# Kernel optimization log

Measured on AMD Instinct MI355X. Metric: run time of the kernel, lower is better.

The kernel has to match this reference:

```python
import jax, jax.numpy as jnp
import numpy as np

TAO, M = 3, 5
C_IN, D_MODEL = 7, 512
KERNELS = D_MODEL // C_IN            # 73
LEFTOUT = D_MODEL - C_IN * KERNELS   # 1
KSIZE = 3
B, L = 32, 4096


def setup_inputs() -> dict:
    key = jax.random.key(0)
    k1, k2, k3, k4, k5 = jax.random.split(key, 5)
    x = jax.random.normal(k1, (B, L, C_IN), dtype=jnp.float32)
    fan_in = (M + 1) * KSIZE
    # kaiming_normal_(mode='fan_in', nonlinearity='leaky_relu', neg_slope=0.01)
    std = float(np.sqrt(2.0 / ((1.0 + 0.01 ** 2) * fan_in)))
    conv_w = jax.random.normal(k2, (KERNELS, M + 1, KSIZE), dtype=jnp.float32) * std
    bb = float(1.0 / np.sqrt(fan_in))  # torch default conv bias init: U(-1/sqrt(fan_in), +)
    conv_b = jax.random.uniform(k3, (KERNELS,), minval=-bb, maxval=bb, dtype=jnp.float32)
    leftout_w = jax.random.normal(k4, (LEFTOUT, M + 1, KSIZE), dtype=jnp.float32) * std
    leftout_b = jax.random.uniform(k5, (LEFTOUT,), minval=-bb, maxval=bb, dtype=jnp.float32)
    return {"x": x, "conv_w": conv_w, "conv_b": conv_b,
            "leftout_w": leftout_w, "leftout_b": leftout_b}


def _circ_conv(inp, w, b):
    # inp: [N, M+1, L]; circular padding=1, kernel 3, 'VALID' after wrap pad
    inp_c = jnp.pad(inp, ((0, 0), (0, 0), (1, 1)), mode="wrap")
    out = jax.lax.conv_general_dilated(
        inp_c, w, window_strides=(1,), padding="VALID",
        dimension_numbers=("NCH", "OIH", "NCH"))
    return out + b[None, :, None]


def reference(x, conv_w, conv_b, leftout_w, leftout_b):
    Bb, Ll, c = x.shape
    off = M * TAO
    # faithful-vector gather: for t in [off, L), take x[t - i*tao, c_], c-major then i
    idx = jnp.arange(off, Ll)[:, None] - jnp.arange(M + 1)[None, :] * TAO  # [L', M+1]
    g = x[:, idx, :]                                   # [B, L', M+1, c]
    g = jnp.transpose(g, (0, 1, 3, 2)).reshape(Bb, Ll - off, c * (M + 1))
    emb = jnp.pad(g, ((0, 0), (off, 0), (0, 0)))       # pad front of seq -> [B, L, c*(M+1)]
    # split into c chunks of (M+1) channels; fold chunk dim into batch for shared conv
    inp = emb.reshape(Bb, Ll, c, M + 1).transpose(0, 2, 3, 1).reshape(Bb * c, M + 1, Ll)
    out = _circ_conv(inp, conv_w, conv_b)              # [B*c, KERNELS, L]
    pieces = out.reshape(Bb, c * KERNELS, Ll)
    if LEFTOUT > 0:
        last = inp.reshape(Bb, c, M + 1, Ll)[:, -1]    # last chunk's conv input [B, M+1, L]
        extra = _circ_conv(last, leftout_w, leftout_b)  # [B, LEFTOUT, L]
        pieces = jnp.concatenate([pieces, extra], axis=1)
    return jnp.transpose(pieces, (0, 2, 1))            # [B, L, d_model]
```

## Files before the change

### kernel.cpp

```cpp
#include <hip/hip_runtime.h>

#define C_IN 7
#define D_MODEL 512
#define KERNELS 73
#define MM 5
#define BBATCH 32
#define LL 4096
#define TCHUNK 72
#define NTAP 18
#define XS_LD (TCHUNK + NTAP)

__global__ __launch_bounds__(512) void tokemb_kernel(
    const float* __restrict__ x, const float* __restrict__ conv_w,
    const float* __restrict__ conv_b, const float* __restrict__ leftout_w,
    const float* __restrict__ leftout_b, float* __restrict__ out)
{
  __shared__ float xs[C_IN * XS_LD];
  const int tid = threadIdx.x;
  const int b = blockIdx.y;
  const int T0 = blockIdx.x * TCHUNK;

  const float* xb = x + (size_t)b * LL * C_IN;
  for (int e = tid; e < C_IN * XS_LD; e += 512) {
    int c = e / XS_LD;
    int q = e - c * XS_LD;
    int p = T0 - 16 + q;
    if (p < 0) p += LL;
    else if (p >= LL) p -= LL;
    xs[e] = xb[p * C_IN + c];
  }

  const int d = tid;
  const bool left = (d == D_MODEL - 1);
  int cc, kk;
  if (left) { cc = C_IN - 1; kk = 0; }
  else { cc = d / KERNELS; kk = d - cc * KERNELS; }
  const float* wsrc = left ? leftout_w : (conv_w + kk * (MM + 1) * 3);
  float wf[NTAP];
  #pragma unroll
  for (int n = 0; n < NTAP; ++n) {
    int m = n / 3, j = 2 - (n % 3);
    wf[n] = wsrc[m * 3 + j];
  }
  const float bias = left ? leftout_b[0] : conv_b[kk];

  __syncthreads();

  const float* xc = xs + cc * XS_LD;

  float win[NTAP];
  #pragma unroll
  for (int p = 0; p < NTAP; ++p) win[p] = xc[p];

  float* outb = out + ((size_t)b * LL + T0) * D_MODEL + d;

  for (int tl0 = 0; tl0 < TCHUNK; tl0 += NTAP) {
    const int tg = T0 + tl0;
    if (tg >= 16 && tg <= LL - 1 - NTAP) {
      #pragma unroll
      for (int u = 0; u < NTAP; ++u) {
        float acc = bias;
        #pragma unroll
        for (int n = 0; n < NTAP; ++n)
          acc += win[(u + 17 - n) % NTAP] * wf[n];
        outb[(size_t)(tl0 + u) * D_MODEL] = acc;
        win[u] = xc[tl0 + u + NTAP];
      }
    } else {
      #pragma unroll
      for (int u = 0; u < NTAP; ++u) {
        const int t = tg + u;
        float acc = bias;
        #pragma unroll
        for (int j = 0; j < 3; ++j) {
          int uu = t - 1 + j;
          if (uu < 0) uu += LL;
          else if (uu >= LL) uu -= LL;
          if (uu >= 15) {
            #pragma unroll
            for (int m = 0; m <= MM; ++m) {
              const int n = 3 * m + 2 - j;
              acc += win[(u + 17 - n) % NTAP] * wf[n];
            }
          }
        }
        if (t < LL) outb[(size_t)(tl0 + u) * D_MODEL] = acc;
        win[u] = xc[tl0 + u + NTAP];
      }
    }
  }
}

extern "C" void kernel_launch(void* const* d_in, const int* in_sizes, int n_in,
                              void* d_out, int out_size, void* d_ws, size_t ws_size,
                              hipStream_t stream) {
  const float* x = (const float*)d_in[0];
  const float* conv_w = (const float*)d_in[1];
  const float* conv_b = (const float*)d_in[2];
  const float* leftout_w = (const float*)d_in[3];
  const float* leftout_b = (const float*)d_in[4];
  float* out = (float*)d_out;
  dim3 grid((LL + TCHUNK - 1) / TCHUNK, BBATCH);
  tokemb_kernel<<<grid, 512, 0, stream>>>(x, conv_w, conv_b, leftout_w, leftout_b, out);
}
```

Measured before the change: 277.7 us.

## Compute two output channels per thread with float2 stores and split time across halves

Each thread now produces two adjacent d_model channels and writes them as one float2 store instead of one scalar store. The 512 threads split into two halves that each cover 18 timesteps of a 36-step chunk, so the block's time tile is halved and the grid doubles. Each thread preloads a full 36-element input window into registers, which removes the rolling reloads from shared memory. This targets store efficiency on an output-write-bound kernel. In exchange it raises register pressure and doubles the overhead of the halo loads.

```diff
diff --git a/kernel.cpp b/kernel.cpp
--- a/kernel.cpp
+++ b/kernel.cpp
@@ -6,9 +6,10 @@
 #define MM 5
 #define BBATCH 32
 #define LL 4096
-#define TCHUNK 72
 #define NTAP 18
+#define TCHUNK 36
 #define XS_LD (TCHUNK + NTAP)
+#define WINW (2 * NTAP)
 
 __global__ __launch_bounds__(512) void tokemb_kernel(
     const float* __restrict__ x, const float* __restrict__ conv_w,
@@ -21,72 +22,80 @@
   const int T0 = blockIdx.x * TCHUNK;
 
   const float* xb = x + (size_t)b * LL * C_IN;
-  for (int e = tid; e < C_IN * XS_LD; e += 512) {
-    int c = e / XS_LD;
-    int q = e - c * XS_LD;
+  if (tid < C_IN * XS_LD) {
+    const int c = tid / XS_LD;
+    const int q = tid - c * XS_LD;
     int p = T0 - 16 + q;
     if (p < 0) p += LL;
     else if (p >= LL) p -= LL;
-    xs[e] = xb[p * C_IN + c];
+    xs[tid] = xb[p * C_IN + c];
   }
 
-  const int d = tid;
-  const bool left = (d == D_MODEL - 1);
-  int cc, kk;
-  if (left) { cc = C_IN - 1; kk = 0; }
-  else { cc = d / KERNELS; kk = d - cc * KERNELS; }
-  const float* wsrc = left ? leftout_w : (conv_w + kk * (MM + 1) * 3);
-  float wf[NTAP];
+  const int dg = tid & 255;
+  const int ts = tid >> 8;
+  const int d0 = dg * 2;
+  const int d1 = d0 + 1;
+  int ccA = d0 / KERNELS;
+  int ccB = d1 / KERNELS; if (ccB > C_IN - 1) ccB = C_IN - 1;
+  const bool leftB = (d1 == D_MODEL - 1);
+  const int kkA = d0 - ccA * KERNELS;
+  const int kkB = leftB ? 0 : (d1 - ccB * KERNELS);
+
+  const float* wA = conv_w + kkA * (MM + 1) * 3;
+  const float* wB = leftB ? leftout_w : (conv_w + kkB * (MM + 1) * 3);
+  float wfA[NTAP], wfB[NTAP];
   #pragma unroll
   for (int n = 0; n < NTAP; ++n) {
-    int m = n / 3, j = 2 - (n % 3);
-    wf[n] = wsrc[m * 3 + j];
+    const int m = n / 3, j = 2 - (n % 3);
+    wfA[n] = wA[m * 3 + j];
+    wfB[n] = wB[m * 3 + j];
   }
-  const float bias = left ? leftout_b[0] : conv_b[kk];
+  const float biasA = conv_b[kkA];
+  const float biasB = leftB ? leftout_b[0] : conv_b[kkB];
 
   __syncthreads();
 
-  const float* xc = xs + cc * XS_LD;
+  const int t0 = T0 + ts * NTAP;
+  const int lbase = ts * NTAP;
+  const float* pA = xs + ccA * XS_LD + lbase;
+  const float* pB = xs + ccB * XS_LD + lbase;
+  float xvA[WINW], xvB[WINW];
+  #pragma unroll
+  for (int i = 0; i < WINW; ++i) { xvA[i] = pA[i]; xvB[i] = pB[i]; }
 
-  float win[NTAP];
-  #pragma unroll
-  for (int p = 0; p < NTAP; ++p) win[p] = xc[p];
+  float2* o = reinterpret_cast<float2*>(out + ((size_t)b * LL + t0) * D_MODEL) + dg;
 
-  float* outb = out + ((size_t)b * LL + T0) * D_MODEL + d;
-
-  for (int tl0 = 0; tl0 < TCHUNK; tl0 += NTAP) {
-    const int tg = T0 + tl0;
-    if (tg >= 16 && tg <= LL - 1 - NTAP) {
+  if (t0 >= 16 && t0 + (NTAP - 1) <= LL - 2) {
+    #pragma unroll
+    for (int u = 0; u < NTAP; ++u) {
+      float a = biasA, c2 = biasB;
       #pragma unroll
-      for (int u = 0; u < NTAP; ++u) {
-        float acc = bias;
-        #pragma unroll
-        for (int n = 0; n < NTAP; ++n)
-          acc += win[(u + 17 - n) % NTAP] * wf[n];
-        outb[(size_t)(tl0 + u) * D_MODEL] = acc;
-        win[u] = xc[tl0 + u + NTAP];
+      for (int n = 0; n < NTAP; ++n) {
+        a  += xvA[u + 17 - n] * wfA[n];
+        c2 += xvB[u + 17 - n] * wfB[n];
       }
-    } else {
+      o[(size_t)u * (D_MODEL / 2)] = make_float2(a, c2);
+    }
+  } else {
+    #pragma unroll
+    for (int u = 0; u < NTAP; ++u) {
+      const int t = t0 + u;
+      float a = biasA, c2 = biasB;
       #pragma unroll
-      for (int u = 0; u < NTAP; ++u) {
-        const int t = tg + u;
-        float acc = bias;
-        #pragma unroll
-        for (int j = 0; j < 3; ++j) {
-          int uu = t - 1 + j;
-          if (uu < 0) uu += LL;
-          else if (uu >= LL) uu -= LL;
-          if (uu >= 15) {
-            #pragma unroll
-            for (int m = 0; m <= MM; ++m) {
-              const int n = 3 * m + 2 - j;
-              acc += win[(u + 17 - n) % NTAP] * wf[n];
-            }
+      for (int j = 0; j < 3; ++j) {
+        int uu = t - 1 + j;
+        if (uu < 0) uu += LL;
+        else if (uu >= LL) uu -= LL;
+        if (uu >= 15) {
+          #pragma unroll
+          for (int m = 0; m <= MM; ++m) {
+            const int n = 3 * m + 2 - j;
+            a  += xvA[u + 17 - n] * wfA[n];
+            c2 += xvB[u + 17 - n] * wfB[n];
           }
         }
-        if (t < LL) outb[(size_t)(tl0 + u) * D_MODEL] = acc;
-        win[u] = xc[tl0 + u + NTAP];
       }
+      if (t < LL) o[(size_t)u * (D_MODEL / 2)] = make_float2(a, c2);
     }
   }
 }
```

Result: slower. 292.7 us (+5.4%).
